# Optimization experiments

Measured on AMD Instinct MI355X. Metric: run time of the kernel, lower is better.

Reference implementation:

```python
import jax, jax.numpy as jnp
import numpy as np
from jax import lax

EPS = 1e-5


def setup_inputs() -> dict:
    key = jax.random.key(0)
    ks = jax.random.split(key, 4)
    B, C, H, W = 8, 256, 64, 64
    G, K = 4, 3
    x = jax.random.normal(ks[0], (B, C, H, W), dtype=jnp.float32)
    # offset/mask branch conv: 3*G*K*K output channels (2 offsets + 1 mask per point)
    w_off = jax.random.normal(ks[1], (3 * G * K * K, C, K, K), dtype=jnp.float32) * 0.01
    b_off = jnp.zeros((3 * G * K * K,), dtype=jnp.float32)
    # deformable conv weight, grouped: [C_out, C_in//G, K, K]
    w_dcn = jax.random.normal(ks[2], (C, C // G, K, K), dtype=jnp.float32) * (1.0 / np.sqrt(C // G * K * K))
    b_dcn = jnp.zeros((C,), dtype=jnp.float32)
    gamma = jnp.ones((C,), dtype=jnp.float32)
    beta = jnp.zeros((C,), dtype=jnp.float32)
    return {"x": x, "w_off": w_off, "b_off": b_off, "w_dcn": w_dcn,
            "b_dcn": b_dcn, "gamma": gamma, "beta": beta}


def _bilinear_gather(flat, idx, valid, B, G, Cg, KK, H, W):
    # flat: [B,G,Cg,H*W]; idx, valid: [B,G,KK,H,W]
    idx_f = idx.reshape(B, G, 1, KK * H * W)
    vals = jnp.take_along_axis(flat, idx_f, axis=3)  # [B,G,Cg,KK*H*W]
    vals = vals.reshape(B, G, Cg, KK, H, W)
    return vals * valid[:, :, None].astype(flat.dtype)


def _dcn_forward(x, w_off, b_off, w_dcn, b_dcn, gamma, beta):
    B, C, H, W = x.shape
    G, K = 4, 3
    KK = K * K
    Cg = C // G
    pad = K // 2
    dn = ("NCHW", "OIHW", "NCHW")

    # offset / modulation branch
    off = lax.conv_general_dilated(x, w_off, (1, 1), "SAME", dimension_numbers=dn)
    off = off + b_off[None, :, None, None]
    offsets = off[:, : 2 * G * KK].reshape(B, G, KK, 2, H, W)
    mask = jax.nn.sigmoid(off[:, 2 * G * KK:]).reshape(B, G, KK, H, W)

    # sampling locations: output pixel + kernel offset + learned offset
    ky, kx = jnp.meshgrid(jnp.arange(K) - pad, jnp.arange(K) - pad, indexing="ij")
    ky = ky.reshape(KK).astype(x.dtype)
    kx = kx.reshape(KK).astype(x.dtype)
    hh = jnp.arange(H, dtype=x.dtype)[:, None]          # [H,1]
    ww = jnp.arange(W, dtype=x.dtype)[None, :]          # [1,W]
    py = hh[None, None, None] + ky[None, None, :, None, None] + offsets[:, :, :, 0]  # [B,G,KK,H,W]
    px = ww[None, None, None] + kx[None, None, :, None, None] + offsets[:, :, :, 1]

    y0 = jnp.floor(py); x0 = jnp.floor(px)
    wy1 = py - y0; wy0 = 1.0 - wy1
    wx1 = px - x0; wx0 = 1.0 - wx1
    y0i = y0.astype(jnp.int32); x0i = x0.astype(jnp.int32)
    y1i = y0i + 1; x1i = x0i + 1

    flat = x.reshape(B, G, Cg, H * W)

    def corner(yi, xi, wgt):
        valid = (yi >= 0) & (yi < H) & (xi >= 0) & (xi < W)
        idx = jnp.clip(yi, 0, H - 1) * W + jnp.clip(xi, 0, W - 1)
        v = _bilinear_gather(flat, idx, valid, B, G, Cg, KK, H, W)
        return v * wgt[:, :, None]

    sampled = (corner(y0i, x0i, wy0 * wx0) + corner(y0i, x1i, wy0 * wx1)
               + corner(y1i, x0i, wy1 * wx0) + corner(y1i, x1i, wy1 * wx1))
    sampled = sampled * mask[:, :, None]                 # [B,G,Cg,KK,H,W]

    wg = w_dcn.reshape(G, C // G, Cg, KK)                # [G, Cout_g, Cin_g, KK]
    out = jnp.einsum("bgckhw,gock->bgohw", sampled, wg).reshape(B, C, H, W)
    out = out + b_dcn[None, :, None, None]

    # LayerNorm over channel dim (applied in BHWC layout)
    a = out.transpose(0, 2, 3, 1)                        # [B,H,W,C]
    mu = jnp.mean(a, axis=-1, keepdims=True)
    var = jnp.mean(jnp.square(a - mu), axis=-1, keepdims=True)
    normed = (a - mu) * lax.rsqrt(var + EPS) * gamma + beta
    attn = jax.nn.sigmoid(normed).transpose(0, 3, 1, 2)  # [B,C,H,W]
    return x * attn


def reference(x, w_off, b_off, w_dcn, b_dcn, gamma, beta):
    return _dcn_forward(x, w_off, b_off, w_dcn, b_dcn, gamma, beta)
```

## Files before the change

### kernel.cpp

```cpp
#include <hip/hip_runtime.h>
#include <math.h>


typedef __attribute__((ext_vector_type(4))) short s16x4;
typedef __attribute__((ext_vector_type(8))) short s16x8;
typedef __attribute__((ext_vector_type(4))) float f32x4;

union S8 { s16x8 v; s16x4 h[2]; };

__device__ __forceinline__ s16x8 ld8(const short* p) {
  S8 r;
  r.h[0] = *(const s16x4*)p;
  r.h[1] = *(const s16x4*)(p + 4);
  return r.v;
}

__device__ __forceinline__ unsigned short bfr(float v) {
  unsigned u = __float_as_uint(v);
  u = (u + 0x7FFFu + ((u >> 16) & 1u)) >> 16;
  return (unsigned short)u;
}
__device__ __forceinline__ float bff(unsigned short s) {
  return __uint_as_float(((unsigned)s) << 16);
}
__device__ __forceinline__ float bf(short s) {
  return __uint_as_float(((unsigned)(unsigned short)s) << 16);
}

__global__ __launch_bounds__(256) void k_prep(
    const float* __restrict__ w_off, const float* __restrict__ w_dcn,
    short* __restrict__ wo_a, short* __restrict__ wd_a) {
  int i = blockIdx.x * 256 + threadIdx.x;
  const int n1 = 112 * 2304;
  if (i < n1) {
    int e = i & 7;
    int t1 = i >> 3;
    int lane = t1 & 63;
    int t2 = t1 >> 6;
    int mt = t2 % 7;
    int t3 = t2 / 7;
    int s = t3 & 1;
    int t4 = t3 >> 1;
    int tap = t4 % 9;
    int part = t4 / 9;
    int co = mt * 16 + (lane & 15);
    int ch = part * 64 + s * 32 + (lane >> 4) * 8 + e;
    float v = (co < 108) ? w_off[(co * 256 + ch) * 9 + tap] : 0.f;
    wo_a[i] = (short)bfr(v);
  } else {
    int j = i - n1;
    int g = j / 36864, r = j % 36864;
    int tap = r >> 12;
    int q = r & 4095;
    int co = q >> 6, cl = q & 63;
    wd_a[j] = (short)bfr(w_dcn[((g * 64 + co) * 64 + cl) * 9 + tap]);
  }
}

__global__ __launch_bounds__(256) void k_x2(
    const float* __restrict__ x, short* __restrict__ x2) {
  int id = blockIdx.x * 256 + threadIdx.x;
  const int n1 = 8 * 32 * 4096;
  if (id < n1) {
    int pc = id & 4095;
    int c2 = (id >> 12) & 31;
    int b = id >> 17;
    int h = pc >> 6, w = pc & 63;
    const float* xp = x + ((size_t)(b * 256 + c2 * 8)) * 4096 + pc;
    short* o = x2 + ((size_t)(b * 32 + c2) * 4356 + (h + 1) * 66 + (w + 1)) * 8;
    s16x4 v0, v1;
#pragma unroll
    for (int i = 0; i < 4; ++i) {
      v0[i] = (short)bfr(xp[(size_t)i * 4096]);
      v1[i] = (short)bfr(xp[(size_t)(i + 4) * 4096]);
    }
    *(s16x4*)o = v0;
    *(s16x4*)(o + 4) = v1;
  } else {
    int j = id - n1;
    int plane = j / 260, r = j % 260;
    int h, w;
    if (r < 66) { h = 0; w = r; }
    else if (r < 132) { h = 65; w = r - 66; }
    else if (r < 196) { h = r - 131; w = 0; }
    else { h = r - 195; w = 65; }
    short* o = x2 + ((size_t)plane * 4356 + h * 66 + w) * 8;
    s16x4 z = {0, 0, 0, 0};
    *(s16x4*)o = z;
    *(s16x4*)(o + 4) = z;
  }
}

__global__ __launch_bounds__(256) void k_offconv(
    const short* __restrict__ x2, const short* __restrict__ wo_a,
    const float* __restrict__ b_off, short* __restrict__ wpart) {
  __shared__ short p_s[4 * 66 * 68];
  int bi = blockIdx.x;
  int xcd = bi & 7;
  int j = bi >> 3;
  int slice = xcd * 4 + (j & 3);
  int h0 = (j >> 2) * 2;
  int part = slice >> 3, b = slice & 7;
  int tid = threadIdx.x;
  int lane = tid & 63, wv = tid >> 6;
  int quad = lane >> 4, l15 = lane & 15;

  f32x4 zero4 = {0.f, 0.f, 0.f, 0.f};
  f32x4 acc[7][2];
#pragma unroll
  for (int i = 0; i < 7; ++i)
#pragma unroll
    for (int r = 0; r < 2; ++r) acc[i][r] = zero4;

  const short* x2b = x2 + (size_t)(b * 32 + part * 8) * 34848;
  const short* wfrag = wo_a + (size_t)part * 64512 + lane * 8;

  for (int it = tid; it < 2112; it += 256) {
    int ck = it / 264;
    int rp = it - ck * 264;
    const short* src = x2b + (size_t)ck * 34848 + ((size_t)h0 * 66 + rp) * 8;
    S8 v;
    v.v = *(const s16x8*)src;
    short* dst = &p_s[rp * 68 + ck * 8];
    *(s16x4*)dst = v.h[0];
    *(s16x4*)(dst + 4) = v.h[1];
  }
  __syncthreads();

  int nb = 16 * wv + l15;
#pragma unroll
  for (int tap = 0; tap < 9; ++tap) {
    int ky = tap / 3, kx = tap % 3;
#pragma unroll
    for (int s = 0; s < 2; ++s) {
      int k0 = 32 * s + quad * 8;
      const short* wb = wfrag + (size_t)(tap * 2 + s) * 3584;
      s16x8 af[7];
#pragma unroll
      for (int mt = 0; mt < 7; ++mt)
        af[mt] = *(const s16x8*)(wb + (size_t)mt * 512);
#pragma unroll
      for (int r = 0; r < 2; ++r) {
        s16x8 bf_f = ld8(&p_s[((r + ky) * 66 + nb + kx) * 68 + k0]);
#pragma unroll
        for (int mt = 0; mt < 7; ++mt)
          acc[mt][r] =
              __builtin_amdgcn_mfma_f32_16x16x32_bf16(af[mt], bf_f, acc[mt][r], 0, 0, 0);
      }
    }
  }

  short* wp = wpart + ((size_t)part * 8 + b) * 108 * 4096;
#pragma unroll
  for (int mt = 0; mt < 7; ++mt) {
#pragma unroll
    for (int rr = 0; rr < 2; ++rr) {
#pragma unroll
      for (int r = 0; r < 4; ++r) {
        int co = 16 * mt + quad * 4 + r;
        if (co < 108) {
          float v = acc[mt][rr][r] + (part == 0 ? b_off[co] : 0.f);
          wp[(size_t)co * 4096 + (h0 + rr) * 64 + nb] = (short)bfr(v);
        }
      }
    }
  }
}

__global__ __launch_bounds__(256) void k_dcn(
    const short* __restrict__ x2, const short* __restrict__ wpart,
    const short* __restrict__ wd_a, const float* __restrict__ b_dcn,
    float* __restrict__ dcn) {
  __shared__ float4 prm[9][64];
  __shared__ short wlds[2][64][72];

  int bi = blockIdx.x;
  int xcd = bi & 7;
  int j = bi >> 3;
  int grp = xcd * 4 + (j & 3);
  int h = j >> 2;
  int b = grp >> 2, g = grp & 3;
  int tid = threadIdx.x;
  int lane = tid & 63, wv = tid >> 6;
  int quad = lane >> 4, l15 = lane & 15;
  int px = 16 * wv + l15;

  f32x4 zero4 = {0.f, 0.f, 0.f, 0.f};
  f32x4 acc[4];
#pragma unroll
  for (int i = 0; i < 4; ++i) acc[i] = zero4;

  const short* x2g = x2 + (size_t)(b * 32 + g * 8) * 34848;
  const short* plA = x2g + (size_t)quad * 34848;
  const short* plB = x2g + (size_t)(quad + 4) * 34848;
  const short* wd_g = wd_a + (size_t)g * 36864;

  int co_w = tid >> 2, kp_w = (tid & 3) * 16;

  {
    const short* wsrc = wd_g + co_w * 64 + kp_w;
    s16x8 w0 = *(const s16x8*)wsrc;
    s16x8 w1 = *(const s16x8*)(wsrc + 8);
    *(s16x8*)&wlds[0][co_w][kp_w] = w0;
    *(s16x8*)&wlds[0][co_w][kp_w + 8] = w1;
  }
  for (int i = tid; i < 576; i += 256) {
    int c = i >> 6, pxa = i & 63;
    int sp = h * 64 + pxa;
    int co_y = (g * 9 + c) * 2;
    float oy = 0.f, ox = 0.f, mz = 0.f;
#pragma unroll
    for (int p4 = 0; p4 < 4; ++p4) {
      const short* wp = wpart + ((size_t)p4 * 8 + b) * 108 * 4096;
      oy += bff((unsigned short)wp[(size_t)co_y * 4096 + sp]);
      ox += bff((unsigned short)wp[(size_t)(co_y + 1) * 4096 + sp]);
      mz += bff((unsigned short)wp[(size_t)(72 + g * 9 + c) * 4096 + sp]);
    }
    float m = 1.f / (1.f + __expf(-mz));
    float py = (float)h + (float)(c / 3 - 1) + oy;
    float pxf = (float)pxa + (float)(c % 3 - 1) + ox;
    prm[c][pxa] = make_float4(py, pxf, m, 0.f);
  }
  __syncthreads();

  s16x8 cA[2][4], cB[2][4];
  float4 wts[2];

  auto stage = [&](int c, int st) {
    float4 pr = prm[c][px];
    float py = pr.x, pxf = pr.y, m = pr.z;
    float y0 = floorf(py), x0 = floorf(pxf);
    float wy1 = py - y0, wy0 = 1.f - wy1;
    float wx1 = pxf - x0, wx0 = 1.f - wx1;
    int y0i = (int)y0, x0i = (int)x0;
    int y1i = y0i + 1, x1i = x0i + 1;
    bool vy0 = (y0i >= 0) & (y0i < 64), vy1 = (y1i >= 0) & (y1i < 64);
    bool vx0 = (x0i >= 0) & (x0i < 64), vx1 = (x1i >= 0) & (x1i < 64);
    int cy0 = min(max(y0i, 0), 63) + 1, cy1 = min(max(y1i, 0), 63) + 1;
    int cx0 = min(max(x0i, 0), 63) + 1, cx1 = min(max(x1i, 0), 63) + 1;
    int i00 = cy0 * 66 + cx0, i01 = cy0 * 66 + cx1;
    int i10 = cy1 * 66 + cx0, i11 = cy1 * 66 + cx1;
    wts[st] = make_float4((vy0 && vx0) ? wy0 * wx0 * m : 0.f,
                          (vy0 && vx1) ? wy0 * wx1 * m : 0.f,
                          (vy1 && vx0) ? wy1 * wx0 * m : 0.f,
                          (vy1 && vx1) ? wy1 * wx1 * m : 0.f);
    cA[st][0] = *(const s16x8*)(plA + (size_t)i00 * 8);
    cA[st][1] = *(const s16x8*)(plA + (size_t)i01 * 8);
    cA[st][2] = *(const s16x8*)(plA + (size_t)i10 * 8);
    cA[st][3] = *(const s16x8*)(plA + (size_t)i11 * 8);
    cB[st][0] = *(const s16x8*)(plB + (size_t)i00 * 8);
    cB[st][1] = *(const s16x8*)(plB + (size_t)i01 * 8);
    cB[st][2] = *(const s16x8*)(plB + (size_t)i10 * 8);
    cB[st][3] = *(const s16x8*)(plB + (size_t)i11 * 8);
  };

  stage(0, 0);
#pragma unroll
  for (int c = 0; c < 9; ++c) {
    int cur = c & 1;
    s16x8 wn0, wn1;
    if (c < 8) {
      const short* wsrc = wd_g + (size_t)(c + 1) * 4096 + co_w * 64 + kp_w;
      wn0 = *(const s16x8*)wsrc;
      wn1 = *(const s16x8*)(wsrc + 8);
      stage(c + 1, cur ^ 1);
    }

    float4 w = wts[cur];
    s16x8 bf0, bf1;
#pragma unroll
    for (int i = 0; i < 8; ++i) {
      float vA = w.x * bf(cA[cur][0][i]) + w.y * bf(cA[cur][1][i]) +
                 w.z * bf(cA[cur][2][i]) + w.w * bf(cA[cur][3][i]);
      float vB = w.x * bf(cB[cur][0][i]) + w.y * bf(cB[cur][1][i]) +
                 w.z * bf(cB[cur][2][i]) + w.w * bf(cB[cur][3][i]);
      bf0[i] = (short)bfr(vA);
      bf1[i] = (short)bfr(vB);
    }

#pragma unroll
    for (int mt = 0; mt < 4; ++mt) {
      s16x8 af = *(const s16x8*)&wlds[cur][16 * mt + l15][quad * 8];
      acc[mt] = __builtin_amdgcn_mfma_f32_16x16x32_bf16(af, bf0, acc[mt], 0, 0, 0);
    }
#pragma unroll
    for (int mt = 0; mt < 4; ++mt) {
      s16x8 af = *(const s16x8*)&wlds[cur][16 * mt + l15][32 + quad * 8];
      acc[mt] = __builtin_amdgcn_mfma_f32_16x16x32_bf16(af, bf1, acc[mt], 0, 0, 0);
    }

    if (c < 8) {
      *(s16x8*)&wlds[cur ^ 1][co_w][kp_w] = wn0;
      *(s16x8*)&wlds[cur ^ 1][co_w][kp_w + 8] = wn1;
      __syncthreads();
    }
  }

  int nb = px;
#pragma unroll
  for (int mt = 0; mt < 4; ++mt) {
#pragma unroll
    for (int r = 0; r < 4; ++r) {
      int co = 16 * mt + quad * 4 + r;
      dcn[(((size_t)b * 256 + g * 64 + co) * 64 + h) * 64 + nb] =
          acc[mt][r] + b_dcn[g * 64 + co];
    }
  }
}

__global__ __launch_bounds__(256) void k_ln(
    const float* __restrict__ dcn, const float* __restrict__ x,
    const float* __restrict__ gamma, const float* __restrict__ beta,
    float* __restrict__ out) {
  __shared__ float red_s[4][64];
  __shared__ float red_q[4][64];
  int px = threadIdx.x & 63;
  int part = threadIdx.x >> 6;
  int p = blockIdx.x * 64 + px;
  int b = p >> 12, hw = p & 4095;
  const float* ob = dcn + (size_t)b * 256 * 4096 + hw;
  const float* xb = x + (size_t)b * 256 * 4096 + hw;
  float* yb = out + (size_t)b * 256 * 4096 + hw;
  int c0 = part * 64;
  float v[64];
  float s = 0.f, s2 = 0.f;
#pragma unroll
  for (int i = 0; i < 64; ++i) {
    v[i] = ob[(c0 + i) * 4096];
    s += v[i];
    s2 += v[i] * v[i];
  }
  red_s[part][px] = s;
  red_q[part][px] = s2;
  __syncthreads();
  s = red_s[0][px] + red_s[1][px] + red_s[2][px] + red_s[3][px];
  s2 = red_q[0][px] + red_q[1][px] + red_q[2][px] + red_q[3][px];
  float mu = s * (1.f / 256.f);
  float var = s2 * (1.f / 256.f) - mu * mu;
  float rs = rsqrtf(var + 1e-5f);
#pragma unroll
  for (int i = 0; i < 64; ++i) {
    int c = c0 + i;
    float nrm = (v[i] - mu) * rs * gamma[c] + beta[c];
    float attn = 1.f / (1.f + __expf(-nrm));
    yb[c * 4096] = xb[c * 4096] * attn;
  }
}

extern "C" void kernel_launch(void* const* d_in, const int* in_sizes, int n_in,
                              void* d_out, int out_size, void* d_ws,
                              size_t ws_size, hipStream_t stream) {
  const float* x = (const float*)d_in[0];
  const float* w_off = (const float*)d_in[1];
  const float* b_off = (const float*)d_in[2];
  const float* w_dcn = (const float*)d_in[3];
  const float* b_dcn = (const float*)d_in[4];
  const float* gamma = (const float*)d_in[5];
  const float* beta = (const float*)d_in[6];
  float* out = (float*)d_out;
  char* wsb = (char*)d_ws;

  short* wpart = (short*)wsb;
  short* wo_a = (short*)(wsb + 28311552);
  short* wd_a = (short*)(wsb + 28827648);
  short* x2 = (short*)(wsb + 29122560);
  float* dcnb = out;

  k_prep<<<1584, 256, 0, stream>>>(w_off, w_dcn, wo_a, wd_a);
  k_x2<<<4356, 256, 0, stream>>>(x, x2);
  k_offconv<<<1024, 256, 0, stream>>>(x2, wo_a, b_off, wpart);
  k_dcn<<<2048, 256, 0, stream>>>(x2, wpart, wd_a, b_dcn, dcnb);
  k_ln<<<512, 256, 0, stream>>>(dcnb, x, gamma, beta, out);
}
```

Baseline: 194.2 us.

## Apply bilinear weights after MFMA per corner and load pre-swizzled DCN weights directly

The DCN kernel no longer blends the four bilinear corners into one bf16 operand before the matrix multiply. It runs a separate MFMA for each corner and scales the fp32 result by that corner's weight. This removes the per-element bf16 interpolation and rounding, at the cost of four times as many MFMAs plus scalar FMAs. The weight prep kernel now writes the DCN weights in MFMA fragment order, so each lane reads its A fragments straight from global memory, dropping the LDS double buffer and the per-tap __syncthreads. Software prefetching of the next tap is also removed, which may expose load latency.

After: 213.4 us. 9.9% more time.

```diff
diff --git a/kernel.cpp b/kernel.cpp
--- a/kernel.cpp
+++ b/kernel.cpp
@@ -50,9 +50,16 @@
   } else {
     int j = i - n1;
     int g = j / 36864, r = j % 36864;
-    int tap = r >> 12;
-    int q = r & 4095;
-    int co = q >> 6, cl = q & 63;
+    int e = r & 7;
+    int t = r >> 3;
+    int lane = t & 63;
+    int t2 = t >> 6;
+    int mt = t2 & 3;
+    int t3 = t2 >> 2;
+    int s = t3 & 1;
+    int tap = t3 >> 1;
+    int co = mt * 16 + (lane & 15);
+    int cl = s * 32 + (lane >> 4) * 8 + e;
     wd_a[j] = (short)bfr(w_dcn[((g * 64 + co) * 64 + cl) * 9 + tap]);
   }
 }
@@ -172,7 +179,6 @@
     const short* __restrict__ wd_a, const float* __restrict__ b_dcn,
     float* __restrict__ dcn) {
   __shared__ float4 prm[9][64];
-  __shared__ short wlds[2][64][72];
 
   int bi = blockIdx.x;
   int xcd = bi & 7;
@@ -193,17 +199,8 @@
   const short* x2g = x2 + (size_t)(b * 32 + g * 8) * 34848;
   const short* plA = x2g + (size_t)quad * 34848;
   const short* plB = x2g + (size_t)(quad + 4) * 34848;
-  const short* wd_g = wd_a + (size_t)g * 36864;
-
-  int co_w = tid >> 2, kp_w = (tid & 3) * 16;
-
-  {
-    const short* wsrc = wd_g + co_w * 64 + kp_w;
-    s16x8 w0 = *(const s16x8*)wsrc;
-    s16x8 w1 = *(const s16x8*)(wsrc + 8);
-    *(s16x8*)&wlds[0][co_w][kp_w] = w0;
-    *(s16x8*)&wlds[0][co_w][kp_w + 8] = w1;
-  }
+  const short* afb = wd_a + (size_t)g * 36864 + lane * 8;
+
   for (int i = tid; i < 576; i += 256) {
     int c = i >> 6, pxa = i & 63;
     int sp = h * 64 + pxa;
@@ -223,10 +220,7 @@
   }
   __syncthreads();
 
-  s16x8 cA[2][4], cB[2][4];
-  float4 wts[2];
-
-  auto stage = [&](int c, int st) {
+  for (int c = 0; c < 9; ++c) {
     float4 pr = prm[c][px];
     float py = pr.x, pxf = pr.y, m = pr.z;
     float y0 = floorf(py), x0 = floorf(pxf);
@@ -240,59 +234,44 @@
     int cx0 = min(max(x0i, 0), 63) + 1, cx1 = min(max(x1i, 0), 63) + 1;
     int i00 = cy0 * 66 + cx0, i01 = cy0 * 66 + cx1;
     int i10 = cy1 * 66 + cx0, i11 = cy1 * 66 + cx1;
-    wts[st] = make_float4((vy0 && vx0) ? wy0 * wx0 * m : 0.f,
-                          (vy0 && vx1) ? wy0 * wx1 * m : 0.f,
-                          (vy1 && vx0) ? wy1 * wx0 * m : 0.f,
-                          (vy1 && vx1) ? wy1 * wx1 * m : 0.f);
-    cA[st][0] = *(const s16x8*)(plA + (size_t)i00 * 8);
-    cA[st][1] = *(const s16x8*)(plA + (size_t)i01 * 8);
-    cA[st][2] = *(const s16x8*)(plA + (size_t)i10 * 8);
-    cA[st][3] = *(const s16x8*)(plA + (size_t)i11 * 8);
-    cB[st][0] = *(const s16x8*)(plB + (size_t)i00 * 8);
-    cB[st][1] = *(const s16x8*)(plB + (size_t)i01 * 8);
-    cB[st][2] = *(const s16x8*)(plB + (size_t)i10 * 8);
-    cB[st][3] = *(const s16x8*)(plB + (size_t)i11 * 8);
-  };
-
-  stage(0, 0);
-#pragma unroll
-  for (int c = 0; c < 9; ++c) {
-    int cur = c & 1;
-    s16x8 wn0, wn1;
-    if (c < 8) {
-      const short* wsrc = wd_g + (size_t)(c + 1) * 4096 + co_w * 64 + kp_w;
-      wn0 = *(const s16x8*)wsrc;
-      wn1 = *(const s16x8*)(wsrc + 8);
-      stage(c + 1, cur ^ 1);
-    }
-
-    float4 w = wts[cur];
-    s16x8 bf0, bf1;
-#pragma unroll
-    for (int i = 0; i < 8; ++i) {
-      float vA = w.x * bf(cA[cur][0][i]) + w.y * bf(cA[cur][1][i]) +
-                 w.z * bf(cA[cur][2][i]) + w.w * bf(cA[cur][3][i]);
-      float vB = w.x * bf(cB[cur][0][i]) + w.y * bf(cB[cur][1][i]) +
-                 w.z * bf(cB[cur][2][i]) + w.w * bf(cB[cur][3][i]);
-      bf0[i] = (short)bfr(vA);
-      bf1[i] = (short)bfr(vB);
-    }
-
+    float wtc[4];
+    wtc[0] = (vy0 && vx0) ? wy0 * wx0 * m : 0.f;
+    wtc[1] = (vy0 && vx1) ? wy0 * wx1 * m : 0.f;
+    wtc[2] = (vy1 && vx0) ? wy1 * wx0 * m : 0.f;
+    wtc[3] = (vy1 && vx1) ? wy1 * wx1 * m : 0.f;
+
+    s16x8 cA[4], cB[4];
+    cA[0] = *(const s16x8*)(plA + (size_t)i00 * 8);
+    cA[1] = *(const s16x8*)(plA + (size_t)i01 * 8);
+    cA[2] = *(const s16x8*)(plA + (size_t)i10 * 8);
+    cA[3] = *(const s16x8*)(plA + (size_t)i11 * 8);
+    cB[0] = *(const s16x8*)(plB + (size_t)i00 * 8);
+    cB[1] = *(const s16x8*)(plB + (size_t)i01 * 8);
+    cB[2] = *(const s16x8*)(plB + (size_t)i10 * 8);
+    cB[3] = *(const s16x8*)(plB + (size_t)i11 * 8);
+
+    const short* wt0 = afb + (size_t)c * 4096;
+    s16x8 af0[4], af1[4];
 #pragma unroll
     for (int mt = 0; mt < 4; ++mt) {
-      s16x8 af = *(const s16x8*)&wlds[cur][16 * mt + l15][quad * 8];
-      acc[mt] = __builtin_amdgcn_mfma_f32_16x16x32_bf16(af, bf0, acc[mt], 0, 0, 0);
-    }
-#pragma unroll
-    for (int mt = 0; mt < 4; ++mt) {
-      s16x8 af = *(const s16x8*)&wlds[cur][16 * mt + l15][32 + quad * 8];
-      acc[mt] = __builtin_amdgcn_mfma_f32_16x16x32_bf16(af, bf1, acc[mt], 0, 0, 0);
-    }
-
-    if (c < 8) {
-      *(s16x8*)&wlds[cur ^ 1][co_w][kp_w] = wn0;
-      *(s16x8*)&wlds[cur ^ 1][co_w][kp_w + 8] = wn1;
-      __syncthreads();
+      af0[mt] = *(const s16x8*)(wt0 + (size_t)mt * 512);
+      af1[mt] = *(const s16x8*)(wt0 + 2048 + (size_t)mt * 512);
+    }
+
+#pragma unroll
+    for (int cr = 0; cr < 4; ++cr) {
+      f32x4 tmp[4];
+#pragma unroll
+      for (int mt = 0; mt < 4; ++mt)
+        tmp[mt] = __builtin_amdgcn_mfma_f32_16x16x32_bf16(af0[mt], cA[cr], zero4, 0, 0, 0);
+#pragma unroll
+      for (int mt = 0; mt < 4; ++mt)
+        tmp[mt] = __builtin_amdgcn_mfma_f32_16x16x32_bf16(af1[mt], cB[cr], tmp[mt], 0, 0, 0);
+      float wc = wtc[cr];
+#pragma unroll
+      for (int mt = 0; mt < 4; ++mt)
+#pragma unroll
+        for (int r = 0; r < 4; ++r) acc[mt][r] += wc * tmp[mt][r];
     }
   }
 
```

## Process two output rows per block in deformable conv to reuse weight tiles

Applied to the files above, without the earlier changes.

Each k_dcn block now computes two output rows instead of one, halving the grid and sharing each staged weight tile in LDS across both rows. The software-pipelined prefetch of the gathered corners for the next tap is removed, and corner loads now happen inline per row. The bf16 packing switches to a paired hardware convert. The block keeps twice the accumulators and loses overlap between the gather and the MFMA work, and with half as many blocks there is less parallelism to hide memory latency.

After: 206.6 us. +6.4%, slower.

```diff
diff --git a/kernel.cpp b/kernel.cpp
--- a/kernel.cpp
+++ b/kernel.cpp
@@ -1,4 +1,5 @@
 #include <hip/hip_runtime.h>
+#include <hip/hip_bf16.h>
 #include <math.h>
 
 
@@ -7,6 +8,7 @@
 typedef __attribute__((ext_vector_type(4))) float f32x4;
 
 union S8 { s16x8 v; s16x4 h[2]; };
+union S8U { s16x8 v; unsigned u[4]; };
 
 __device__ __forceinline__ s16x8 ld8(const short* p) {
   S8 r;
@@ -25,6 +27,11 @@
 }
 __device__ __forceinline__ float bf(short s) {
   return __uint_as_float(((unsigned)(unsigned short)s) << 16);
+}
+__device__ __forceinline__ unsigned cvtpk(float lo, float hi) {
+  union { __hip_bfloat162 b; unsigned u; } cv;
+  cv.b = __float22bfloat162_rn(make_float2(lo, hi));
+  return cv.u;
 }
 
 __global__ __launch_bounds__(256) void k_prep(
@@ -171,14 +178,14 @@
     const short* __restrict__ x2, const short* __restrict__ wpart,
     const short* __restrict__ wd_a, const float* __restrict__ b_dcn,
     float* __restrict__ dcn) {
-  __shared__ float4 prm[9][64];
+  __shared__ float4 prm[9][2][64];
   __shared__ short wlds[2][64][72];
 
   int bi = blockIdx.x;
   int xcd = bi & 7;
   int j = bi >> 3;
   int grp = xcd * 4 + (j & 3);
-  int h = j >> 2;
+  int h0 = (j >> 2) * 2;
   int b = grp >> 2, g = grp & 3;
   int tid = threadIdx.x;
   int lane = tid & 63, wv = tid >> 6;
@@ -186,9 +193,11 @@
   int px = 16 * wv + l15;
 
   f32x4 zero4 = {0.f, 0.f, 0.f, 0.f};
-  f32x4 acc[4];
-#pragma unroll
-  for (int i = 0; i < 4; ++i) acc[i] = zero4;
+  f32x4 acc[2][4];
+#pragma unroll
+  for (int r = 0; r < 2; ++r)
+#pragma unroll
+    for (int i = 0; i < 4; ++i) acc[r][i] = zero4;
 
   const short* x2g = x2 + (size_t)(b * 32 + g * 8) * 34848;
   const short* plA = x2g + (size_t)quad * 34848;
@@ -204,9 +213,12 @@
     *(s16x8*)&wlds[0][co_w][kp_w] = w0;
     *(s16x8*)&wlds[0][co_w][kp_w + 8] = w1;
   }
-  for (int i = tid; i < 576; i += 256) {
-    int c = i >> 6, pxa = i & 63;
-    int sp = h * 64 + pxa;
+  for (int i = tid; i < 1152; i += 256) {
+    int c = i >> 7;
+    int rem = i & 127;
+    int rr = rem >> 6;
+    int pxa = rem & 63;
+    int sp = (h0 + rr) * 64 + pxa;
     int co_y = (g * 9 + c) * 2;
     float oy = 0.f, ox = 0.f, mz = 0.f;
 #pragma unroll
@@ -217,44 +229,12 @@
       mz += bff((unsigned short)wp[(size_t)(72 + g * 9 + c) * 4096 + sp]);
     }
     float m = 1.f / (1.f + __expf(-mz));
-    float py = (float)h + (float)(c / 3 - 1) + oy;
+    float py = (float)(h0 + rr) + (float)(c / 3 - 1) + oy;
     float pxf = (float)pxa + (float)(c % 3 - 1) + ox;
-    prm[c][pxa] = make_float4(py, pxf, m, 0.f);
+    prm[c][rr][pxa] = make_float4(py, pxf, m, 0.f);
   }
   __syncthreads();
 
-  s16x8 cA[2][4], cB[2][4];
-  float4 wts[2];
-
-  auto stage = [&](int c, int st) {
-    float4 pr = prm[c][px];
-    float py = pr.x, pxf = pr.y, m = pr.z;
-    float y0 = floorf(py), x0 = floorf(pxf);
-    float wy1 = py - y0, wy0 = 1.f - wy1;
-    float wx1 = pxf - x0, wx0 = 1.f - wx1;
-    int y0i = (int)y0, x0i = (int)x0;
-    int y1i = y0i + 1, x1i = x0i + 1;
-    bool vy0 = (y0i >= 0) & (y0i < 64), vy1 = (y1i >= 0) & (y1i < 64);
-    bool vx0 = (x0i >= 0) & (x0i < 64), vx1 = (x1i >= 0) & (x1i < 64);
-    int cy0 = min(max(y0i, 0), 63) + 1, cy1 = min(max(y1i, 0), 63) + 1;
-    int cx0 = min(max(x0i, 0), 63) + 1, cx1 = min(max(x1i, 0), 63) + 1;
-    int i00 = cy0 * 66 + cx0, i01 = cy0 * 66 + cx1;
-    int i10 = cy1 * 66 + cx0, i11 = cy1 * 66 + cx1;
-    wts[st] = make_float4((vy0 && vx0) ? wy0 * wx0 * m : 0.f,
-                          (vy0 && vx1) ? wy0 * wx1 * m : 0.f,
-                          (vy1 && vx0) ? wy1 * wx0 * m : 0.f,
-                          (vy1 && vx1) ? wy1 * wx1 * m : 0.f);
-    cA[st][0] = *(const s16x8*)(plA + (size_t)i00 * 8);
-    cA[st][1] = *(const s16x8*)(plA + (size_t)i01 * 8);
-    cA[st][2] = *(const s16x8*)(plA + (size_t)i10 * 8);
-    cA[st][3] = *(const s16x8*)(plA + (size_t)i11 * 8);
-    cB[st][0] = *(const s16x8*)(plB + (size_t)i00 * 8);
-    cB[st][1] = *(const s16x8*)(plB + (size_t)i01 * 8);
-    cB[st][2] = *(const s16x8*)(plB + (size_t)i10 * 8);
-    cB[st][3] = *(const s16x8*)(plB + (size_t)i11 * 8);
-  };
-
-  stage(0, 0);
 #pragma unroll
   for (int c = 0; c < 9; ++c) {
     int cur = c & 1;
@@ -263,30 +243,63 @@
       const short* wsrc = wd_g + (size_t)(c + 1) * 4096 + co_w * 64 + kp_w;
       wn0 = *(const s16x8*)wsrc;
       wn1 = *(const s16x8*)(wsrc + 8);
-      stage(c + 1, cur ^ 1);
-    }
-
-    float4 w = wts[cur];
-    s16x8 bf0, bf1;
-#pragma unroll
-    for (int i = 0; i < 8; ++i) {
-      float vA = w.x * bf(cA[cur][0][i]) + w.y * bf(cA[cur][1][i]) +
-                 w.z * bf(cA[cur][2][i]) + w.w * bf(cA[cur][3][i]);
-      float vB = w.x * bf(cB[cur][0][i]) + w.y * bf(cB[cur][1][i]) +
-                 w.z * bf(cB[cur][2][i]) + w.w * bf(cB[cur][3][i]);
-      bf0[i] = (short)bfr(vA);
-      bf1[i] = (short)bfr(vB);
-    }
-
-#pragma unroll
-    for (int mt = 0; mt < 4; ++mt) {
-      s16x8 af = *(const s16x8*)&wlds[cur][16 * mt + l15][quad * 8];
-      acc[mt] = __builtin_amdgcn_mfma_f32_16x16x32_bf16(af, bf0, acc[mt], 0, 0, 0);
-    }
-#pragma unroll
-    for (int mt = 0; mt < 4; ++mt) {
-      s16x8 af = *(const s16x8*)&wlds[cur][16 * mt + l15][32 + quad * 8];
-      acc[mt] = __builtin_amdgcn_mfma_f32_16x16x32_bf16(af, bf1, acc[mt], 0, 0, 0);
+    }
+
+#pragma unroll
+    for (int rr = 0; rr < 2; ++rr) {
+      float4 pr = prm[c][rr][px];
+      float py = pr.x, pxf = pr.y, m = pr.z;
+      float y0 = floorf(py), x0 = floorf(pxf);
+      float wy1 = py - y0, wy0 = 1.f - wy1;
+      float wx1 = pxf - x0, wx0 = 1.f - wx1;
+      int y0i = (int)y0, x0i = (int)x0;
+      int y1i = y0i + 1, x1i = x0i + 1;
+      bool vy0 = (y0i >= 0) & (y0i < 64), vy1 = (y1i >= 0) & (y1i < 64);
+      bool vx0 = (x0i >= 0) & (x0i < 64), vx1 = (x1i >= 0) & (x1i < 64);
+      int cy0 = min(max(y0i, 0), 63) + 1, cy1 = min(max(y1i, 0), 63) + 1;
+      int cx0 = min(max(x0i, 0), 63) + 1, cx1 = min(max(x1i, 0), 63) + 1;
+      int i00 = cy0 * 66 + cx0, i01 = cy0 * 66 + cx1;
+      int i10 = cy1 * 66 + cx0, i11 = cy1 * 66 + cx1;
+      float w00 = (vy0 && vx0) ? wy0 * wx0 * m : 0.f;
+      float w01 = (vy0 && vx1) ? wy0 * wx1 * m : 0.f;
+      float w10 = (vy1 && vx0) ? wy1 * wx0 * m : 0.f;
+      float w11 = (vy1 && vx1) ? wy1 * wx1 * m : 0.f;
+
+      s16x8 a00 = *(const s16x8*)(plA + (size_t)i00 * 8);
+      s16x8 a01 = *(const s16x8*)(plA + (size_t)i01 * 8);
+      s16x8 a10 = *(const s16x8*)(plA + (size_t)i10 * 8);
+      s16x8 a11 = *(const s16x8*)(plA + (size_t)i11 * 8);
+      s16x8 b00 = *(const s16x8*)(plB + (size_t)i00 * 8);
+      s16x8 b01 = *(const s16x8*)(plB + (size_t)i01 * 8);
+      s16x8 b10 = *(const s16x8*)(plB + (size_t)i10 * 8);
+      s16x8 b11 = *(const s16x8*)(plB + (size_t)i11 * 8);
+
+      S8U bf0, bf1;
+#pragma unroll
+      for (int i2 = 0; i2 < 4; ++i2) {
+        int e0 = 2 * i2, e1 = 2 * i2 + 1;
+        float vA0 = w00 * bf(a00[e0]) + w01 * bf(a01[e0]) +
+                    w10 * bf(a10[e0]) + w11 * bf(a11[e0]);
+        float vA1 = w00 * bf(a00[e1]) + w01 * bf(a01[e1]) +
+                    w10 * bf(a10[e1]) + w11 * bf(a11[e1]);
+        float vB0 = w00 * bf(b00[e0]) + w01 * bf(b01[e0]) +
+                    w10 * bf(b10[e0]) + w11 * bf(b11[e0]);
+        float vB1 = w00 * bf(b00[e1]) + w01 * bf(b01[e1]) +
+                    w10 * bf(b10[e1]) + w11 * bf(b11[e1]);
+        bf0.u[i2] = cvtpk(vA0, vA1);
+        bf1.u[i2] = cvtpk(vB0, vB1);
+      }
+
+#pragma unroll
+      for (int mt = 0; mt < 4; ++mt) {
+        s16x8 af = *(const s16x8*)&wlds[cur][16 * mt + l15][quad * 8];
+        acc[rr][mt] = __builtin_amdgcn_mfma_f32_16x16x32_bf16(af, bf0.v, acc[rr][mt], 0, 0, 0);
+      }
+#pragma unroll
+      for (int mt = 0; mt < 4; ++mt) {
+        s16x8 af = *(const s16x8*)&wlds[cur][16 * mt + l15][32 + quad * 8];
+        acc[rr][mt] = __builtin_amdgcn_mfma_f32_16x16x32_bf16(af, bf1.v, acc[rr][mt], 0, 0, 0);
+      }
     }
 
     if (c < 8) {
@@ -298,12 +311,15 @@
 
   int nb = px;
 #pragma unroll
-  for (int mt = 0; mt < 4; ++mt) {
-#pragma unroll
-    for (int r = 0; r < 4; ++r) {
-      int co = 16 * mt + quad * 4 + r;
-      dcn[(((size_t)b * 256 + g * 64 + co) * 64 + h) * 64 + nb] =
-          acc[mt][r] + b_dcn[g * 64 + co];
+  for (int rr = 0; rr < 2; ++rr) {
+#pragma unroll
+    for (int mt = 0; mt < 4; ++mt) {
+#pragma unroll
+      for (int r = 0; r < 4; ++r) {
+        int co = 16 * mt + quad * 4 + r;
+        dcn[(((size_t)b * 256 + g * 64 + co) * 64 + (h0 + rr)) * 64 + nb] =
+            acc[rr][mt][r] + b_dcn[g * 64 + co];
+      }
     }
   }
 }
@@ -369,6 +385,6 @@
   k_prep<<<1584, 256, 0, stream>>>(w_off, w_dcn, wo_a, wd_a);
   k_x2<<<4356, 256, 0, stream>>>(x, x2);
   k_offconv<<<1024, 256, 0, stream>>>(x2, wo_a, b_off, wpart);
-  k_dcn<<<2048, 256, 0, stream>>>(x2, wpart, wd_a, b_dcn, dcnb);
+  k_dcn<<<1024, 256, 0, stream>>>(x2, wpart, wd_a, b_dcn, dcnb);
   k_ln<<<512, 256, 0, stream>>>(dcnb, x, gamma, beta, out);
 }
```
